# Kernel tuning notes

Hardware: AMD Instinct MI355X
Metric: run time of the kernel (lower is better)

The kernel has to match this reference:

```python
import jax, jax.numpy as jnp
import numpy as np

B, T, C = 8, 1024, 1024
H, HS = 16, 64            # n_head, head_size
K, STRIDE = 32, 16        # block_length, stride_length
WIN = 128                 # local_window_size
EPS = 1e-5


def _ln(z, w):
    m = jnp.mean(z, axis=-1, keepdims=True)
    v = jnp.var(z, axis=-1, keepdims=True)
    return (z - m) / jnp.sqrt(v + EPS) * w


def setup_inputs() -> dict:
    key = jax.random.key(0)
    ks = jax.random.split(key, 8)
    s = 0.02
    return {
        "x": jax.random.normal(ks[0], (B, T, C), jnp.float32),
        "c_attn_w": jax.random.normal(ks[1], (3 * C, C), jnp.float32) * s,
        "conv_w": jax.random.normal(ks[2], (HS, HS, K), jnp.float32) * s,
        "ln_comp_w": jnp.ones((HS,), jnp.float32),
        "ln_local_w": jnp.ones((C,), jnp.float32),
        "gate_w1": jax.random.normal(ks[3], (C, 2 * C), jnp.float32) * s,
        "gate_ln_w": jnp.ones((C,), jnp.float32),
        "gate_w2": jax.random.normal(ks[4], (2, C), jnp.float32) * s,
        "c_proj_w": jax.random.normal(ks[5], (C, C), jnp.float32) * s,
    }


def reference(x, c_attn_w, conv_w, ln_comp_w, ln_local_w, gate_w1, gate_ln_w, gate_w2, c_proj_w):
    qkv = jnp.einsum('btc,oc->bto', x, c_attn_w)          # [B,T,3C]
    q, k, v = jnp.split(qkv, 3, axis=-1)
    def heads(t):
        return t.reshape(B, T, H, HS).transpose(0, 2, 1, 3)  # [B,H,T,hs]
    q, k, v = heads(q), heads(k), heads(v)

    # CompressionMLP: Conv1d over time + LayerNorm(hs) + exact GELU
    def compress(t):
        xr = t.transpose(0, 1, 3, 2).reshape(B * H, HS, T)   # [B*H, hs, T]
        co = jax.lax.conv_general_dilated(
            xr, conv_w, window_strides=(STRIDE,), padding='VALID',
            dimension_numbers=('NCH', 'OIH', 'NCH'))          # [B*H, hs, NB]
        co = co.transpose(0, 2, 1)                            # [B*H, NB, hs]
        co = jax.nn.gelu(_ln(co, ln_comp_w), approximate=False)
        nb = co.shape[1]
        return co.reshape(B, H, nb, HS)

    kc = compress(k)
    vc = compress(v)
    NB = kc.shape[2]  # 63
    scale = 1.0 / np.sqrt(HS)

    ti = jnp.arange(T)
    band = (ti[None, :] <= ti[:, None]) & (ti[None, :] >= ti[:, None] - WIN)  # [T,T]
    s_loc = jnp.einsum('bhqd,bhkd->bhqk', q, k) * scale
    s_loc = jnp.where(band[None, None], s_loc, -jnp.inf)
    local_out = jnp.einsum('bhqk,bhkd->bhqd', jax.nn.softmax(s_loc, axis=-1), v)
    local_out = local_out.transpose(0, 2, 1, 3).reshape(B, T, C)
    local_norm = _ln(local_out, ln_local_w)

    # compressed-KV attention with block-causal mask: block j <= token i
    bj = jnp.arange(NB)
    cmask = bj[None, :] <= ti[:, None]                        # [T,NB]
    s_cmp = jnp.einsum('bhqd,bhkd->bhqk', q, kc) * scale
    s_cmp = jnp.where(cmask[None, None], s_cmp, -jnp.inf)
    comp_out = jnp.einsum('bhqk,bhkd->bhqd', jax.nn.softmax(s_cmp, axis=-1), vc)
    comp_out = comp_out.transpose(0, 2, 1, 3).reshape(B, T, C)

    # AttentionGating: last-token features -> Linear -> LN -> ReLU -> Linear -> softmax
    feats = jnp.concatenate([local_norm[:, -1, :], comp_out[:, -1, :]], axis=-1)  # [B,2C]
    h = jax.nn.relu(_ln(feats @ gate_w1.T, gate_ln_w))
    gates = jax.nn.softmax(h @ gate_w2.T, axis=-1)            # [B,2]

    combined = gates[:, None, 0:1] * local_norm + gates[:, None, 1:2] * comp_out
    y = jnp.einsum('btc,oc->bto', combined, c_proj_w)
    return y
```

## Files before the change

### kernel.cpp

```cpp
#include <hip/hip_runtime.h>
#include <cstdint>
#include <cmath>
#include <cstddef>

typedef unsigned int u32;
typedef unsigned short u16;
typedef __bf16 bf16x8 __attribute__((ext_vector_type(8)));
typedef float f32x4 __attribute__((ext_vector_type(4)));
typedef u32 u32x4 __attribute__((ext_vector_type(4)));
typedef u32 u32x2 __attribute__((ext_vector_type(2)));

#define DEV static __device__ __forceinline__

DEV u16 f2bf(float f) {
  u32 u = __float_as_uint(f);
  u += 0x7fffu + ((u >> 16) & 1u);
  return (u16)(u >> 16);
}
DEV float wredsum(float v) {
#pragma unroll
  for (int o = 32; o; o >>= 1) v += __shfl_xor(v, o, 64);
  return v;
}

DEV void gload_lds16(const u16* g, u16* lds_base) {
  __builtin_amdgcn_global_load_lds((const __attribute__((address_space(1))) void*)g,
                                   (__attribute__((address_space(3))) void*)lds_base,
                                   16, 0, 0);
}

__global__ __launch_bounds__(256) void cast_f32_bf16(const float* __restrict__ in,
                                                     u16* __restrict__ out) {
  const size_t idx = ((size_t)blockIdx.x * 256 + threadIdx.x) * 4;
  const f32x4 v = *(const f32x4*)&in[idx];
  u32x2 r;
  r[0] = (u32)f2bf(v[0]) | ((u32)f2bf(v[1]) << 16);
  r[1] = (u32)f2bf(v[2]) | ((u32)f2bf(v[3]) << 16);
  *(u32x2*)&out[idx] = r;
}

__global__ __launch_bounds__(256) void cast_convw(const float* __restrict__ cw,
                                                  u16* __restrict__ wc) {
  const int idx = blockIdx.x * 256 + threadIdx.x;
  const int o = idx >> 11;
  const int rest = idx & 2047;
  const int i = rest >> 5;
  const int kk = rest & 31;
  wc[(o << 11) + (kk << 6) + i] = f2bf(cw[idx]);
}

template <int OUT_BF16>
__global__ __launch_bounds__(256) void gemm_bt(const u16* __restrict__ A,
                                               const u16* __restrict__ Bm,
                                               void* __restrict__ out,
                                               int M, int N, int K) {
  __shared__ u16 As[128 * 32];
  __shared__ u16 Bs[128 * 32];
  const int tid = threadIdx.x;
  const int lane = tid & 63;
  const int w = tid >> 6;
  const int row0 = blockIdx.x * 128;
  const int col0 = blockIdx.y * 128;
  const int wm = (w >> 1) * 64, wn = (w & 1) * 64;
  const int lr = lane & 15, lq = lane >> 4;
  const int srow = lane >> 2;
  const int scol = (lane & 3) * 8;

  f32x4 acc[4][4] = {};

  for (int k0 = 0; k0 < K; k0 += 32) {
    __syncthreads();
#pragma unroll
    for (int p = 0; p < 2; ++p) {
      const int base_r = p * 64 + w * 16;
      gload_lds16(&A[(size_t)(row0 + base_r + srow) * K + k0 + scol], &As[base_r * 32]);
      gload_lds16(&Bm[(size_t)(col0 + base_r + srow) * K + k0 + scol], &Bs[base_r * 32]);
    }
    __syncthreads();
    bf16x8 af[4], bfr[4];
#pragma unroll
    for (int i = 0; i < 4; ++i) {
      af[i] = *(const bf16x8*)&As[(wm + i * 16 + lr) * 32 + lq * 8];
      bfr[i] = *(const bf16x8*)&Bs[(wn + i * 16 + lr) * 32 + lq * 8];
    }
#pragma unroll
    for (int i = 0; i < 4; ++i)
#pragma unroll
      for (int j = 0; j < 4; ++j)
        acc[i][j] = __builtin_amdgcn_mfma_f32_16x16x32_bf16(af[i], bfr[j], acc[i][j], 0, 0, 0);
  }
#pragma unroll
  for (int i = 0; i < 4; ++i)
#pragma unroll
    for (int j = 0; j < 4; ++j)
#pragma unroll
      for (int rr = 0; rr < 4; ++rr) {
        const int gr = row0 + wm + i * 16 + lq * 4 + rr;
        const int gc = col0 + wn + j * 16 + lr;
        const float v = acc[i][j][rr];
        if (OUT_BF16)
          ((u16*)out)[(size_t)gr * N + gc] = f2bf(v);
        else
          ((float*)out)[(size_t)gr * N + gc] = v;
      }
}

__global__ __launch_bounds__(256) void compress_kernel(const u16* __restrict__ qkv,
                                                       const u16* __restrict__ Wc,
                                                       const float* __restrict__ ln_w,
                                                       float* __restrict__ out_k,
                                                       float* __restrict__ out_v) {
  __shared__ u16 As[128 * 32];
  __shared__ u16 Bs[64 * 32];
  __shared__ float Cs[128][65];
  const int srcoff = 1024 + (int)blockIdx.y * 1024;
  float* outp = blockIdx.y ? out_v : out_k;
  const int tid = threadIdx.x;
  const int lane = tid & 63;
  const int w = tid >> 6;
  const int r0 = blockIdx.x * 128;
  const int lr = lane & 15, lq = lane >> 4;

  size_t rowbase[2];
#pragma unroll
  for (int p = 0; p < 2; ++p) {
    const int idx = p * 256 + tid;
    const int r = idx >> 2, c = (idx & 3) * 8;
    const int gr = r0 + r;
    const int bh = gr / 63;
    const int nb = gr - bh * 63;
    const int b = bh >> 4, h = bh & 15;
    rowbase[p] = (size_t)(b * 1024 + nb * 16) * 3072 + srcoff + h * 64 + c;
  }
  const int brow = tid >> 2, bcol = (tid & 3) * 8;

  f32x4 acc[2][4] = {};
  for (int k0 = 0; k0 < 2048; k0 += 32) {
    const int kk = k0 >> 6;
    const int i0 = k0 & 63;
    __syncthreads();
#pragma unroll
    for (int p = 0; p < 2; ++p) {
      const int idx = p * 256 + tid;
      const int r = idx >> 2, c = (idx & 3) * 8;
      *(u32x4*)&As[r * 32 + c] = *(const u32x4*)&qkv[rowbase[p] + (size_t)kk * 3072 + i0];
    }
    *(u32x4*)&Bs[brow * 32 + bcol] = *(const u32x4*)&Wc[(size_t)brow * 2048 + k0 + bcol];
    __syncthreads();
    bf16x8 af[2], bfr[4];
#pragma unroll
    for (int i = 0; i < 2; ++i) af[i] = *(const bf16x8*)&As[(w * 32 + i * 16 + lr) * 32 + lq * 8];
#pragma unroll
    for (int j = 0; j < 4; ++j) bfr[j] = *(const bf16x8*)&Bs[(j * 16 + lr) * 32 + lq * 8];
#pragma unroll
    for (int i = 0; i < 2; ++i)
#pragma unroll
      for (int j = 0; j < 4; ++j)
        acc[i][j] = __builtin_amdgcn_mfma_f32_16x16x32_bf16(af[i], bfr[j], acc[i][j], 0, 0, 0);
  }
  __syncthreads();
#pragma unroll
  for (int i = 0; i < 2; ++i)
#pragma unroll
    for (int j = 0; j < 4; ++j)
#pragma unroll
      for (int rr = 0; rr < 4; ++rr)
        Cs[w * 32 + i * 16 + lq * 4 + rr][j * 16 + lr] = acc[i][j][rr];
  __syncthreads();
  if (tid < 128) {
    const int r = tid;
    float s = 0.f, s2 = 0.f;
#pragma unroll 8
    for (int d = 0; d < 64; ++d) {
      const float x = Cs[r][d];
      s += x;
      s2 += x * x;
    }
    const float m = s * (1.f / 64.f);
    const float inv = rsqrtf(s2 * (1.f / 64.f) - m * m + 1e-5f);
    const size_t gr = (size_t)(r0 + r) * 64;
#pragma unroll 8
    for (int d = 0; d < 64; ++d) {
      const float z = (Cs[r][d] - m) * inv * ln_w[d];
      outp[gr + d] = 0.5f * z * (1.f + erff(z * 0.70710678118f));
    }
  }
}

__global__ __launch_bounds__(256) void local_attn(const u16* __restrict__ qkv,
                                                  float* __restrict__ loc) {
  __shared__ __align__(16) char smem[53248];
  u16* Ks = (u16*)smem;
  u16* Vt = (u16*)smem;
  u16* Ps = (u16*)(smem + 27648);
  const int bh = blockIdx.x;
  const int b = bh >> 4, h = bh & 15;
  const int i0 = blockIdx.y * 64;
  const int jbase = i0 - 128;
  const int tid = threadIdx.x;
  const int lane = tid & 63, w = tid >> 6;
  const int lr = lane & 15, lq = lane >> 4;

  u32x4 vreg[6];
#pragma unroll
  for (int c = 0; c < 6; ++c) {
    const int lin = c * 256 + tid;
    const int s = lin >> 3, d0 = (lin & 7) * 8;
    const int j = jbase + s;
    u32x4 kval = {0, 0, 0, 0}, vval = {0, 0, 0, 0};
    if (j >= 0) {
      const size_t ro = (size_t)(b * 1024 + j) * 3072 + h * 64 + d0;
      kval = *(const u32x4*)&qkv[ro + 1024];
      vval = *(const u32x4*)&qkv[ro + 2048];
    }
    vreg[c] = vval;
    *(u32x4*)&Ks[s * 72 + d0] = kval;
  }
  bf16x8 qf[2];
  {
    const size_t qrow = (size_t)(b * 1024 + i0 + w * 16 + lr) * 3072 + h * 64;
#pragma unroll
    for (int ks = 0; ks < 2; ++ks) qf[ks] = *(const bf16x8*)&qkv[qrow + ks * 32 + lq * 8];
  }
  __syncthreads();

  f32x4 sa[12];
#pragma unroll
  for (int j = 0; j < 12; ++j) sa[j] = (f32x4){0.f, 0.f, 0.f, 0.f};
#pragma unroll
  for (int ks = 0; ks < 2; ++ks)
#pragma unroll
    for (int j = 0; j < 12; ++j) {
      const bf16x8 kf = *(const bf16x8*)&Ks[(j * 16 + lr) * 72 + ks * 32 + lq * 8];
      sa[j] = __builtin_amdgcn_mfma_f32_16x16x32_bf16(qf[ks], kf, sa[j], 0, 0, 0);
    }

  const float NINF = -__builtin_inff();
  float mx[4] = {NINF, NINF, NINF, NINF};
#pragma unroll
  for (int j = 0; j < 12; ++j) {
    const int s = j * 16 + lr;
#pragma unroll
    for (int rr = 0; rr < 4; ++rr) {
      const int qi = w * 16 + lq * 4 + rr;
      const bool valid = (jbase + s >= 0) && (s >= qi) && (s <= qi + 128);
      const float v = valid ? sa[j][rr] * 0.125f : NINF;
      sa[j][rr] = v;
      mx[rr] = fmaxf(mx[rr], v);
    }
  }
#pragma unroll
  for (int rr = 0; rr < 4; ++rr)
#pragma unroll
    for (int o = 1; o < 16; o <<= 1) mx[rr] = fmaxf(mx[rr], __shfl_xor(mx[rr], o, 64));
  float sum[4] = {0.f, 0.f, 0.f, 0.f};
#pragma unroll
  for (int j = 0; j < 12; ++j)
#pragma unroll
    for (int rr = 0; rr < 4; ++rr) {
      const float p = __expf(sa[j][rr] - mx[rr]);
      sa[j][rr] = p;
      sum[rr] += p;
    }
#pragma unroll
  for (int rr = 0; rr < 4; ++rr) {
#pragma unroll
    for (int o = 1; o < 16; o <<= 1) sum[rr] += __shfl_xor(sum[rr], o, 64);
    sum[rr] = 1.0f / sum[rr];
  }
  __syncthreads();

#pragma unroll
  for (int j = 0; j < 12; ++j)
#pragma unroll
    for (int rr = 0; rr < 4; ++rr)
      Ps[(w * 16 + lq * 4 + rr) * 200 + j * 16 + lr] = f2bf(sa[j][rr] * sum[rr]);
#pragma unroll
  for (int c = 0; c < 6; ++c) {
    const int lin = c * 256 + tid;
    const int s = lin >> 3, d0 = (lin & 7) * 8;
    const u32x4 val = vreg[c];
#pragma unroll
    for (int q = 0; q < 4; ++q) {
      Vt[(d0 + 2 * q) * 200 + s] = (u16)(val[q] & 0xffffu);
      Vt[(d0 + 2 * q + 1) * 200 + s] = (u16)(val[q] >> 16);
    }
  }
  __syncthreads();

  f32x4 oa[4];
#pragma unroll
  for (int jt = 0; jt < 4; ++jt) oa[jt] = (f32x4){0.f, 0.f, 0.f, 0.f};
#pragma unroll
  for (int ks = 0; ks < 6; ++ks) {
    const bf16x8 pf = *(const bf16x8*)&Ps[(w * 16 + lr) * 200 + ks * 32 + lq * 8];
#pragma unroll
    for (int jt = 0; jt < 4; ++jt) {
      const bf16x8 vf = *(const bf16x8*)&Vt[(jt * 16 + lr) * 200 + ks * 32 + lq * 8];
      oa[jt] = __builtin_amdgcn_mfma_f32_16x16x32_bf16(pf, vf, oa[jt], 0, 0, 0);
    }
  }
#pragma unroll
  for (int jt = 0; jt < 4; ++jt)
#pragma unroll
    for (int rr = 0; rr < 4; ++rr)
      loc[(size_t)(b * 1024 + i0 + w * 16 + lq * 4 + rr) * 1024 + h * 64 + jt * 16 + lr] =
          oa[jt][rr];
}

__global__ __launch_bounds__(256) void comp_attn(const u16* __restrict__ qkv,
                                                 const float* __restrict__ kc,
                                                 const float* __restrict__ vc,
                                                 float* __restrict__ outc) {
  __shared__ u16 Kc[64 * 72];
  __shared__ u16 Vt[64 * 72];
  __shared__ u16 Ps[64 * 72];
  const int bh = blockIdx.x;
  const int b = bh >> 4, h = bh & 15;
  const int i0 = blockIdx.y * 64;
  const int tid = threadIdx.x;
  const int lane = tid & 63, w = tid >> 6;
  const int lr = lane & 15, lq = lane >> 4;
  const size_t kbase = (size_t)bh * 63 * 64;

  for (int idx = tid; idx < 63 * 64; idx += 256) {
    const int j = idx >> 6, d = idx & 63;
    Kc[j * 72 + d] = f2bf(kc[kbase + idx]);
    Vt[d * 72 + j] = f2bf(vc[kbase + idx]);
  }
  if (tid < 64) {
    Kc[63 * 72 + tid] = 0;
    Vt[tid * 72 + 63] = 0;
  }
  bf16x8 qf[2];
  {
    const size_t qrow = (size_t)(b * 1024 + i0 + w * 16 + lr) * 3072 + h * 64;
#pragma unroll
    for (int ks = 0; ks < 2; ++ks) qf[ks] = *(const bf16x8*)&qkv[qrow + ks * 32 + lq * 8];
  }
  __syncthreads();

  f32x4 sa[4];
#pragma unroll
  for (int j = 0; j < 4; ++j) sa[j] = (f32x4){0.f, 0.f, 0.f, 0.f};
#pragma unroll
  for (int ks = 0; ks < 2; ++ks)
#pragma unroll
    for (int j = 0; j < 4; ++j) {
      const bf16x8 kf = *(const bf16x8*)&Kc[(j * 16 + lr) * 72 + ks * 32 + lq * 8];
      sa[j] = __builtin_amdgcn_mfma_f32_16x16x32_bf16(qf[ks], kf, sa[j], 0, 0, 0);
    }

  const float NINF = -__builtin_inff();
  float mx[4] = {NINF, NINF, NINF, NINF};
#pragma unroll
  for (int j = 0; j < 4; ++j) {
    const int s = j * 16 + lr;
#pragma unroll
    for (int rr = 0; rr < 4; ++rr) {
      const int i = i0 + w * 16 + lq * 4 + rr;
      const bool valid = (s <= i) && (s < 63);
      const float v = valid ? sa[j][rr] * 0.125f : NINF;
      sa[j][rr] = v;
      mx[rr] = fmaxf(mx[rr], v);
    }
  }
#pragma unroll
  for (int rr = 0; rr < 4; ++rr)
#pragma unroll
    for (int o = 1; o < 16; o <<= 1) mx[rr] = fmaxf(mx[rr], __shfl_xor(mx[rr], o, 64));
  float sum[4] = {0.f, 0.f, 0.f, 0.f};
#pragma unroll
  for (int j = 0; j < 4; ++j)
#pragma unroll
    for (int rr = 0; rr < 4; ++rr) {
      const float p = __expf(sa[j][rr] - mx[rr]);
      sa[j][rr] = p;
      sum[rr] += p;
    }
#pragma unroll
  for (int rr = 0; rr < 4; ++rr) {
#pragma unroll
    for (int o = 1; o < 16; o <<= 1) sum[rr] += __shfl_xor(sum[rr], o, 64);
    sum[rr] = 1.0f / sum[rr];
  }
#pragma unroll
  for (int j = 0; j < 4; ++j)
#pragma unroll
    for (int rr = 0; rr < 4; ++rr)
      Ps[(w * 16 + lq * 4 + rr) * 72 + j * 16 + lr] = f2bf(sa[j][rr] * sum[rr]);
  __syncthreads();

  f32x4 oa[4];
#pragma unroll
  for (int jt = 0; jt < 4; ++jt) oa[jt] = (f32x4){0.f, 0.f, 0.f, 0.f};
#pragma unroll
  for (int ks = 0; ks < 2; ++ks) {
    const bf16x8 pf = *(const bf16x8*)&Ps[(w * 16 + lr) * 72 + ks * 32 + lq * 8];
#pragma unroll
    for (int jt = 0; jt < 4; ++jt) {
      const bf16x8 vf = *(const bf16x8*)&Vt[(jt * 16 + lr) * 72 + ks * 32 + lq * 8];
      oa[jt] = __builtin_amdgcn_mfma_f32_16x16x32_bf16(pf, vf, oa[jt], 0, 0, 0);
    }
  }
#pragma unroll
  for (int jt = 0; jt < 4; ++jt)
#pragma unroll
    for (int rr = 0; rr < 4; ++rr)
      outc[(size_t)(b * 1024 + i0 + w * 16 + lq * 4 + rr) * 1024 + h * 64 + jt * 16 + lr] =
          oa[jt][rr];
}

__global__ __launch_bounds__(256) void ln_feats(const float* __restrict__ locn,
                                                const float* __restrict__ comp,
                                                const float* __restrict__ lnw,
                                                float* __restrict__ feats) {
  const int b = blockIdx.x, tid = threadIdx.x;
  const size_t base = ((size_t)b * 1024 + 1023) * 1024 + tid * 4;
  const f32x4 v = *(const f32x4*)&locn[base];
  float s = v[0] + v[1] + v[2] + v[3];
  float s2 = v[0] * v[0] + v[1] * v[1] + v[2] * v[2] + v[3] * v[3];
  s = wredsum(s);
  s2 = wredsum(s2);
  __shared__ float rs[4], rs2[4];
  const int w = tid >> 6, lane = tid & 63;
  if (!lane) { rs[w] = s; rs2[w] = s2; }
  __syncthreads();
  s = rs[0] + rs[1] + rs[2] + rs[3];
  s2 = rs2[0] + rs2[1] + rs2[2] + rs2[3];
  const float m = s * (1.f / 1024.f);
  const float inv = rsqrtf(s2 * (1.f / 1024.f) - m * m + 1e-5f);
  const f32x4 wv = *(const f32x4*)&lnw[tid * 4];
  f32x4 o;
#pragma unroll
  for (int k = 0; k < 4; ++k) o[k] = (v[k] - m) * inv * wv[k];
  *(f32x4*)&feats[b * 2048 + tid * 4] = o;
  *(f32x4*)&feats[b * 2048 + 1024 + tid * 4] = *(const f32x4*)&comp[base];
}

__global__ __launch_bounds__(256) void gate_gemv(const float* __restrict__ feats,
                                                 const float* __restrict__ w1,
                                                 float* __restrict__ hraw) {
  const int o = blockIdx.x * 4 + (threadIdx.x >> 6);
  const int lane = threadIdx.x & 63;
  const float* wr = &w1[(size_t)o * 2048];
  float acc[8] = {};
#pragma unroll
  for (int it = 0; it < 8; ++it) {
    const int c = (it * 64 + lane) * 4;
    const f32x4 wv = *(const f32x4*)&wr[c];
#pragma unroll
    for (int b = 0; b < 8; ++b) {
      const f32x4 fv = *(const f32x4*)&feats[b * 2048 + c];
      acc[b] += fv[0] * wv[0] + fv[1] * wv[1] + fv[2] * wv[2] + fv[3] * wv[3];
    }
  }
#pragma unroll
  for (int b = 0; b < 8; ++b) acc[b] = wredsum(acc[b]);
  if (lane == 0) {
#pragma unroll
    for (int b = 0; b < 8; ++b) hraw[b * 1024 + o] = acc[b];
  }
}

__global__ __launch_bounds__(256) void gate_fin(const float* __restrict__ hraw,
                                                const float* __restrict__ lnw,
                                                const float* __restrict__ w2,
                                                float* __restrict__ gates) {
  const int b = blockIdx.x, tid = threadIdx.x;
  const f32x4 v = *(const f32x4*)&hraw[(size_t)b * 1024 + tid * 4];
  float s = v[0] + v[1] + v[2] + v[3];
  float s2 = v[0] * v[0] + v[1] * v[1] + v[2] * v[2] + v[3] * v[3];
  s = wredsum(s);
  s2 = wredsum(s2);
  __shared__ float rs[4], rs2[4];
  const int w = tid >> 6, lane = tid & 63;
  if (!lane) { rs[w] = s; rs2[w] = s2; }
  __syncthreads();
  s = rs[0] + rs[1] + rs[2] + rs[3];
  s2 = rs2[0] + rs2[1] + rs2[2] + rs2[3];
  const float m = s * (1.f / 1024.f);
  const float inv = rsqrtf(s2 * (1.f / 1024.f) - m * m + 1e-5f);
  float p0 = 0.f, p1 = 0.f;
#pragma unroll
  for (int k = 0; k < 4; ++k) {
    float hh = (v[k] - m) * inv * lnw[tid * 4 + k];
    hh = fmaxf(hh, 0.f);
    p0 += hh * w2[tid * 4 + k];
    p1 += hh * w2[1024 + tid * 4 + k];
  }
  p0 = wredsum(p0);
  p1 = wredsum(p1);
  __syncthreads();
  if (!lane) { rs[w] = p0; rs2[w] = p1; }
  __syncthreads();
  if (tid == 0) {
    const float l0 = rs[0] + rs[1] + rs[2] + rs[3];
    const float l1 = rs2[0] + rs2[1] + rs2[2] + rs2[3];
    const float mm = fmaxf(l0, l1);
    const float e0 = __expf(l0 - mm), e1 = __expf(l1 - mm);
    const float iv = 1.f / (e0 + e1);
    gates[b * 2] = e0 * iv;
    gates[b * 2 + 1] = e1 * iv;
  }
}

__global__ __launch_bounds__(256) void combine_ln_cast(const float* __restrict__ locn,
                                                       const float* __restrict__ comp,
                                                       const float* __restrict__ lnw,
                                                       const float* __restrict__ gates,
                                                       u16* __restrict__ outb) {
  const int row = blockIdx.x, tid = threadIdx.x;
  const size_t base = (size_t)row * 1024 + tid * 4;
  const f32x4 v = *(const f32x4*)&locn[base];
  float s = v[0] + v[1] + v[2] + v[3];
  float s2 = v[0] * v[0] + v[1] * v[1] + v[2] * v[2] + v[3] * v[3];
  s = wredsum(s);
  s2 = wredsum(s2);
  __shared__ float rs[4], rs2[4];
  const int w = tid >> 6, lane = tid & 63;
  if (!lane) { rs[w] = s; rs2[w] = s2; }
  __syncthreads();
  s = rs[0] + rs[1] + rs[2] + rs[3];
  s2 = rs2[0] + rs2[1] + rs2[2] + rs2[3];
  const float m = s * (1.f / 1024.f);
  const float inv = rsqrtf(s2 * (1.f / 1024.f) - m * m + 1e-5f);
  const int b = row >> 10;
  const float g0 = gates[2 * b], g1 = gates[2 * b + 1];
  const f32x4 wv = *(const f32x4*)&lnw[tid * 4];
  const f32x4 c = *(const f32x4*)&comp[base];
  float ov[4];
#pragma unroll
  for (int k = 0; k < 4; ++k) ov[k] = g0 * ((v[k] - m) * inv * wv[k]) + g1 * c[k];
  u32x2 r;
  r[0] = (u32)f2bf(ov[0]) | ((u32)f2bf(ov[1]) << 16);
  r[1] = (u32)f2bf(ov[2]) | ((u32)f2bf(ov[3]) << 16);
  *(u32x2*)&outb[base] = r;
}

extern "C" void kernel_launch(void* const* d_in, const int* in_sizes, int n_in,
                              void* d_out, int out_size, void* d_ws, size_t ws_size,
                              hipStream_t stream) {
  const float* x = (const float*)d_in[0];
  const float* c_attn_w = (const float*)d_in[1];
  const float* conv_w = (const float*)d_in[2];
  const float* ln_comp_w = (const float*)d_in[3];
  const float* ln_local_w = (const float*)d_in[4];
  const float* gate_w1 = (const float*)d_in[5];
  const float* gate_ln_w = (const float*)d_in[6];
  const float* gate_w2 = (const float*)d_in[7];
  const float* c_proj_w = (const float*)d_in[8];
  float* y = (float*)d_out;

  char* ws = (char*)d_ws;
  size_t off = 0;
  auto alloc = [&](size_t bytes) -> void* {
    void* p = ws + off;
    off += (bytes + 255) & ~(size_t)255;
    return p;
  };
  u16* qkvb = (u16*)alloc((size_t)8192 * 3072 * 2);
  u16* xb = (u16*)alloc((size_t)8192 * 1024 * 2);
  u16* wab = (u16*)alloc((size_t)3072 * 1024 * 2);
  u16* wpb = (u16*)alloc((size_t)1024 * 1024 * 2);
  u16* wcb = (u16*)alloc((size_t)64 * 2048 * 2);
  float* kc = (float*)alloc((size_t)8064 * 64 * 4);
  float* vc = (float*)alloc((size_t)8064 * 64 * 4);
  float* locn = (float*)alloc((size_t)8192 * 1024 * 4);
  float* comp = (float*)alloc((size_t)8192 * 1024 * 4);
  float* feats = (float*)alloc((size_t)8 * 2048 * 4);
  float* hraw = (float*)alloc((size_t)8192 * 4);
  float* gates = (float*)alloc(64);
  u16* combb = (u16*)alloc((size_t)8192 * 1024 * 2);

  cast_f32_bf16<<<8192, 256, 0, stream>>>(x, xb);
  cast_f32_bf16<<<3072, 256, 0, stream>>>(c_attn_w, wab);
  cast_f32_bf16<<<1024, 256, 0, stream>>>(c_proj_w, wpb);
  cast_convw<<<512, 256, 0, stream>>>(conv_w, wcb);

  gemm_bt<1><<<dim3(64, 24), 256, 0, stream>>>(xb, wab, qkvb, 8192, 3072, 1024);

  compress_kernel<<<dim3(63, 2), 256, 0, stream>>>(qkvb, wcb, ln_comp_w, kc, vc);

  local_attn<<<dim3(128, 16), 256, 0, stream>>>(qkvb, locn);
  comp_attn<<<dim3(128, 16), 256, 0, stream>>>(qkvb, kc, vc, comp);

  ln_feats<<<8, 256, 0, stream>>>(locn, comp, ln_local_w, feats);
  gate_gemv<<<256, 256, 0, stream>>>(feats, gate_w1, hraw);
  gate_fin<<<8, 256, 0, stream>>>(hraw, gate_ln_w, gate_w2, gates);

  combine_ln_cast<<<8192, 256, 0, stream>>>(locn, comp, ln_local_w, gates, combb);

  gemm_bt<0><<<dim3(64, 8), 256, 0, stream>>>(combb, wpb, y, 8192, 1024, 1024);
}
```

Before: 333.0 us.

## Fuse local and compressed attention, store intermediates in bf16, skip masked tiles

Merges the four cast kernels into one launch, which also zero-pads the compressed K/V buffers. The compress kernel now writes bf16 compressed K and transposed V directly. The local and compressed attention kernels are fused so each block reuses its Q fragments. The local score loop computes only the 9 key tiles inside each wave's band instead of 12, and the PV loop does 5 k-steps instead of 6. Local and compressed attention outputs are stored as bf16 instead of fp32, which halves traffic into the gating and combine kernels at some cost in precision.

```diff
diff --git a/kernel.cpp b/kernel.cpp
--- a/kernel.cpp
+++ b/kernel.cpp
@@ -12,11 +12,16 @@
 
 #define DEV static __device__ __forceinline__
 
+DEV float bflo(u32 u) { return __uint_as_float(u << 16); }
+DEV float bfhi(u32 u) { return __uint_as_float(u & 0xffff0000u); }
 DEV u16 f2bf(float f) {
   u32 u = __float_as_uint(f);
   u += 0x7fffu + ((u >> 16) & 1u);
   return (u16)(u >> 16);
 }
+DEV f32x4 unpack_bf4(u32x2 r) {
+  return (f32x4){bflo(r[0]), bfhi(r[0]), bflo(r[1]), bfhi(r[1])};
+}
 DEV float wredsum(float v) {
 #pragma unroll
   for (int o = 32; o; o >>= 1) v += __shfl_xor(v, o, 64);
@@ -29,24 +34,44 @@
                                    16, 0, 0);
 }
 
-__global__ __launch_bounds__(256) void cast_f32_bf16(const float* __restrict__ in,
-                                                     u16* __restrict__ out) {
-  const size_t idx = ((size_t)blockIdx.x * 256 + threadIdx.x) * 4;
-  const f32x4 v = *(const f32x4*)&in[idx];
-  u32x2 r;
-  r[0] = (u32)f2bf(v[0]) | ((u32)f2bf(v[1]) << 16);
-  r[1] = (u32)f2bf(v[2]) | ((u32)f2bf(v[3]) << 16);
-  *(u32x2*)&out[idx] = r;
-}
-
-__global__ __launch_bounds__(256) void cast_convw(const float* __restrict__ cw,
-                                                  u16* __restrict__ wc) {
-  const int idx = blockIdx.x * 256 + threadIdx.x;
-  const int o = idx >> 11;
-  const int rest = idx & 2047;
-  const int i = rest >> 5;
-  const int kk = rest & 31;
-  wc[(o << 11) + (kk << 6) + i] = f2bf(cw[idx]);
+__global__ __launch_bounds__(256) void fused_cast(const float* __restrict__ x,
+                                                  const float* __restrict__ aw,
+                                                  const float* __restrict__ pw,
+                                                  const float* __restrict__ cw,
+                                                  u16* __restrict__ xb,
+                                                  u16* __restrict__ wab,
+                                                  u16* __restrict__ wpb,
+                                                  u16* __restrict__ wcb,
+                                                  u16* __restrict__ kcb,
+                                                  u16* __restrict__ vcb) {
+  const int blk = blockIdx.x;
+  if (blk < 12288) {
+    const float* src;
+    u16* dst;
+    int base;
+    if (blk < 8192) { src = x; dst = xb; base = blk; }
+    else if (blk < 11264) { src = aw; dst = wab; base = blk - 8192; }
+    else { src = pw; dst = wpb; base = blk - 11264; }
+    const size_t idx = ((size_t)base * 256 + threadIdx.x) * 4;
+    const f32x4 v = *(const f32x4*)&src[idx];
+    u32x2 r;
+    r[0] = (u32)f2bf(v[0]) | ((u32)f2bf(v[1]) << 16);
+    r[1] = (u32)f2bf(v[2]) | ((u32)f2bf(v[3]) << 16);
+    *(u32x2*)&dst[idx] = r;
+  } else if (blk < 12800) {
+    const int idx = (blk - 12288) * 256 + threadIdx.x;
+    const int o = idx >> 11;
+    const int rest = idx & 2047;
+    const int i = rest >> 5;
+    const int kk = rest & 31;
+    wcb[(o << 11) + (kk << 6) + i] = f2bf(cw[idx]);
+  } else {
+    for (int i = threadIdx.x; i < 8192; i += 256) {
+      const int bh = i >> 6, d = i & 63;
+      kcb[bh * 4096 + 63 * 64 + d] = 0;
+      vcb[bh * 4096 + d * 64 + 63] = 0;
+    }
+  }
 }
 
 template <int OUT_BF16>
@@ -108,13 +133,12 @@
 __global__ __launch_bounds__(256) void compress_kernel(const u16* __restrict__ qkv,
                                                        const u16* __restrict__ Wc,
                                                        const float* __restrict__ ln_w,
-                                                       float* __restrict__ out_k,
-                                                       float* __restrict__ out_v) {
+                                                       u16* __restrict__ kcb,
+                                                       u16* __restrict__ vcb) {
   __shared__ u16 As[128 * 32];
   __shared__ u16 Bs[64 * 32];
   __shared__ float Cs[128][65];
   const int srcoff = 1024 + (int)blockIdx.y * 1024;
-  float* outp = blockIdx.y ? out_v : out_k;
   const int tid = threadIdx.x;
   const int lane = tid & 63;
   const int w = tid >> 6;
@@ -169,26 +193,41 @@
   __syncthreads();
   if (tid < 128) {
     const int r = tid;
+    const int gr = r0 + r;
+    const int bh2 = gr / 63;
+    const int nb2 = gr - bh2 * 63;
     float s = 0.f, s2 = 0.f;
 #pragma unroll 8
     for (int d = 0; d < 64; ++d) {
-      const float x = Cs[r][d];
-      s += x;
-      s2 += x * x;
+      const float xv = Cs[r][d];
+      s += xv;
+      s2 += xv * xv;
     }
     const float m = s * (1.f / 64.f);
     const float inv = rsqrtf(s2 * (1.f / 64.f) - m * m + 1e-5f);
-    const size_t gr = (size_t)(r0 + r) * 64;
+    if (blockIdx.y == 0) {
+      const size_t gb = (size_t)bh2 * 4096 + nb2 * 64;
 #pragma unroll 8
-    for (int d = 0; d < 64; ++d) {
-      const float z = (Cs[r][d] - m) * inv * ln_w[d];
-      outp[gr + d] = 0.5f * z * (1.f + erff(z * 0.70710678118f));
-    }
-  }
-}
-
-__global__ __launch_bounds__(256) void local_attn(const u16* __restrict__ qkv,
-                                                  float* __restrict__ loc) {
+      for (int d = 0; d < 64; ++d) {
+        const float z = (Cs[r][d] - m) * inv * ln_w[d];
+        kcb[gb + d] = f2bf(0.5f * z * (1.f + erff(z * 0.70710678118f)));
+      }
+    } else {
+      const size_t gb = (size_t)bh2 * 4096 + nb2;
+#pragma unroll 8
+      for (int d = 0; d < 64; ++d) {
+        const float z = (Cs[r][d] - m) * inv * ln_w[d];
+        vcb[gb + d * 64] = f2bf(0.5f * z * (1.f + erff(z * 0.70710678118f)));
+      }
+    }
+  }
+}
+
+__global__ __launch_bounds__(256) void attn_fused(const u16* __restrict__ qkv,
+                                                  const u16* __restrict__ kcb,
+                                                  const u16* __restrict__ vcb,
+                                                  u16* __restrict__ loc,
+                                                  u16* __restrict__ outc) {
   __shared__ __align__(16) char smem[53248];
   u16* Ks = (u16*)smem;
   u16* Vt = (u16*)smem;
@@ -224,28 +263,29 @@
   }
   __syncthreads();
 
-  f32x4 sa[12];
-#pragma unroll
-  for (int j = 0; j < 12; ++j) sa[j] = (f32x4){0.f, 0.f, 0.f, 0.f};
+  f32x4 sa[9];
+#pragma unroll
+  for (int j9 = 0; j9 < 9; ++j9) sa[j9] = (f32x4){0.f, 0.f, 0.f, 0.f};
 #pragma unroll
   for (int ks = 0; ks < 2; ++ks)
 #pragma unroll
-    for (int j = 0; j < 12; ++j) {
-      const bf16x8 kf = *(const bf16x8*)&Ks[(j * 16 + lr) * 72 + ks * 32 + lq * 8];
-      sa[j] = __builtin_amdgcn_mfma_f32_16x16x32_bf16(qf[ks], kf, sa[j], 0, 0, 0);
+    for (int j9 = 0; j9 < 9; ++j9) {
+      const int jt = w + j9;
+      const bf16x8 kf = *(const bf16x8*)&Ks[(jt * 16 + lr) * 72 + ks * 32 + lq * 8];
+      sa[j9] = __builtin_amdgcn_mfma_f32_16x16x32_bf16(qf[ks], kf, sa[j9], 0, 0, 0);
     }
 
   const float NINF = -__builtin_inff();
   float mx[4] = {NINF, NINF, NINF, NINF};
 #pragma unroll
-  for (int j = 0; j < 12; ++j) {
-    const int s = j * 16 + lr;
+  for (int j9 = 0; j9 < 9; ++j9) {
+    const int s = (w + j9) * 16 + lr;
 #pragma unroll
     for (int rr = 0; rr < 4; ++rr) {
       const int qi = w * 16 + lq * 4 + rr;
       const bool valid = (jbase + s >= 0) && (s >= qi) && (s <= qi + 128);
-      const float v = valid ? sa[j][rr] * 0.125f : NINF;
-      sa[j][rr] = v;
+      const float v = valid ? sa[j9][rr] * 0.125f : NINF;
+      sa[j9][rr] = v;
       mx[rr] = fmaxf(mx[rr], v);
     }
   }
@@ -255,11 +295,11 @@
     for (int o = 1; o < 16; o <<= 1) mx[rr] = fmaxf(mx[rr], __shfl_xor(mx[rr], o, 64));
   float sum[4] = {0.f, 0.f, 0.f, 0.f};
 #pragma unroll
-  for (int j = 0; j < 12; ++j)
+  for (int j9 = 0; j9 < 9; ++j9)
 #pragma unroll
     for (int rr = 0; rr < 4; ++rr) {
-      const float p = __expf(sa[j][rr] - mx[rr]);
-      sa[j][rr] = p;
+      const float p = __expf(sa[j9][rr] - mx[rr]);
+      sa[j9][rr] = p;
       sum[rr] += p;
     }
 #pragma unroll
@@ -271,10 +311,17 @@
   __syncthreads();
 
 #pragma unroll
-  for (int j = 0; j < 12; ++j)
+  for (int j9 = 0; j9 < 9; ++j9) {
+    const int jt = w + j9;
 #pragma unroll
     for (int rr = 0; rr < 4; ++rr)
-      Ps[(w * 16 + lq * 4 + rr) * 200 + j * 16 + lr] = f2bf(sa[j][rr] * sum[rr]);
+      Ps[(w * 16 + lq * 4 + rr) * 200 + jt * 16 + lr] = f2bf(sa[j9][rr] * sum[rr]);
+  }
+  {
+    const int jz = (w == 0) ? 9 : (w == 1) ? 0 : (w == 2) ? 11 : 2;
+#pragma unroll
+    for (int rr = 0; rr < 4; ++rr) Ps[(w * 16 + lq * 4 + rr) * 200 + jz * 16 + lr] = 0;
+  }
 #pragma unroll
   for (int c = 0; c < 6; ++c) {
     const int lin = c * 256 + tid;
@@ -288,15 +335,16 @@
   }
   __syncthreads();
 
+  const int W = (w >> 1) * 32;
   f32x4 oa[4];
 #pragma unroll
   for (int jt = 0; jt < 4; ++jt) oa[jt] = (f32x4){0.f, 0.f, 0.f, 0.f};
 #pragma unroll
-  for (int ks = 0; ks < 6; ++ks) {
-    const bf16x8 pf = *(const bf16x8*)&Ps[(w * 16 + lr) * 200 + ks * 32 + lq * 8];
+  for (int ks = 0; ks < 5; ++ks) {
+    const bf16x8 pf = *(const bf16x8*)&Ps[(w * 16 + lr) * 200 + W + ks * 32 + lq * 8];
 #pragma unroll
     for (int jt = 0; jt < 4; ++jt) {
-      const bf16x8 vf = *(const bf16x8*)&Vt[(jt * 16 + lr) * 200 + ks * 32 + lq * 8];
+      const bf16x8 vf = *(const bf16x8*)&Vt[(jt * 16 + lr) * 200 + W + ks * 32 + lq * 8];
       oa[jt] = __builtin_amdgcn_mfma_f32_16x16x32_bf16(pf, vf, oa[jt], 0, 0, 0);
     }
   }
@@ -305,54 +353,34 @@
 #pragma unroll
     for (int rr = 0; rr < 4; ++rr)
       loc[(size_t)(b * 1024 + i0 + w * 16 + lq * 4 + rr) * 1024 + h * 64 + jt * 16 + lr] =
-          oa[jt][rr];
-}
-
-__global__ __launch_bounds__(256) void comp_attn(const u16* __restrict__ qkv,
-                                                 const float* __restrict__ kc,
-                                                 const float* __restrict__ vc,
-                                                 float* __restrict__ outc) {
-  __shared__ u16 Kc[64 * 72];
-  __shared__ u16 Vt[64 * 72];
-  __shared__ u16 Ps[64 * 72];
-  const int bh = blockIdx.x;
-  const int b = bh >> 4, h = bh & 15;
-  const int i0 = blockIdx.y * 64;
-  const int tid = threadIdx.x;
-  const int lane = tid & 63, w = tid >> 6;
-  const int lr = lane & 15, lq = lane >> 4;
-  const size_t kbase = (size_t)bh * 63 * 64;
-
-  for (int idx = tid; idx < 63 * 64; idx += 256) {
-    const int j = idx >> 6, d = idx & 63;
-    Kc[j * 72 + d] = f2bf(kc[kbase + idx]);
-    Vt[d * 72 + j] = f2bf(vc[kbase + idx]);
-  }
-  if (tid < 64) {
-    Kc[63 * 72 + tid] = 0;
-    Vt[tid * 72 + 63] = 0;
-  }
-  bf16x8 qf[2];
-  {
-    const size_t qrow = (size_t)(b * 1024 + i0 + w * 16 + lr) * 3072 + h * 64;
-#pragma unroll
-    for (int ks = 0; ks < 2; ++ks) qf[ks] = *(const bf16x8*)&qkv[qrow + ks * 32 + lq * 8];
-  }
-  __syncthreads();
-
-  f32x4 sa[4];
-#pragma unroll
-  for (int j = 0; j < 4; ++j) sa[j] = (f32x4){0.f, 0.f, 0.f, 0.f};
+          f2bf(oa[jt][rr]);
+
+  __syncthreads();
+  u16* Kc = (u16*)smem;
+  u16* Vc = (u16*)(smem + 9216);
+  u16* Pc = (u16*)(smem + 18432);
+  const size_t cb = (size_t)bh * 4096;
+  for (int c2 = tid; c2 < 512; c2 += 256) {
+    const int nb = c2 >> 3, d0 = (c2 & 7) * 8;
+    *(u32x4*)&Kc[nb * 72 + d0] = *(const u32x4*)&kcb[cb + nb * 64 + d0];
+  }
+  for (int c2 = tid; c2 < 512; c2 += 256) {
+    const int d = c2 >> 3, n0 = (c2 & 7) * 8;
+    *(u32x4*)&Vc[d * 72 + n0] = *(const u32x4*)&vcb[cb + d * 64 + n0];
+  }
+  __syncthreads();
+
+  f32x4 ca[4];
+#pragma unroll
+  for (int j = 0; j < 4; ++j) ca[j] = (f32x4){0.f, 0.f, 0.f, 0.f};
 #pragma unroll
   for (int ks = 0; ks < 2; ++ks)
 #pragma unroll
     for (int j = 0; j < 4; ++j) {
       const bf16x8 kf = *(const bf16x8*)&Kc[(j * 16 + lr) * 72 + ks * 32 + lq * 8];
-      sa[j] = __builtin_amdgcn_mfma_f32_16x16x32_bf16(qf[ks], kf, sa[j], 0, 0, 0);
-    }
-
-  const float NINF = -__builtin_inff();
-  float mx[4] = {NINF, NINF, NINF, NINF};
+      ca[j] = __builtin_amdgcn_mfma_f32_16x16x32_bf16(qf[ks], kf, ca[j], 0, 0, 0);
+    }
+  float mc[4] = {NINF, NINF, NINF, NINF};
 #pragma unroll
   for (int j = 0; j < 4; ++j) {
     const int s = j * 16 + lr;
@@ -360,47 +388,47 @@
     for (int rr = 0; rr < 4; ++rr) {
       const int i = i0 + w * 16 + lq * 4 + rr;
       const bool valid = (s <= i) && (s < 63);
-      const float v = valid ? sa[j][rr] * 0.125f : NINF;
-      sa[j][rr] = v;
-      mx[rr] = fmaxf(mx[rr], v);
+      const float v = valid ? ca[j][rr] * 0.125f : NINF;
+      ca[j][rr] = v;
+      mc[rr] = fmaxf(mc[rr], v);
     }
   }
 #pragma unroll
   for (int rr = 0; rr < 4; ++rr)
 #pragma unroll
-    for (int o = 1; o < 16; o <<= 1) mx[rr] = fmaxf(mx[rr], __shfl_xor(mx[rr], o, 64));
-  float sum[4] = {0.f, 0.f, 0.f, 0.f};
+    for (int o = 1; o < 16; o <<= 1) mc[rr] = fmaxf(mc[rr], __shfl_xor(mc[rr], o, 64));
+  float sc[4] = {0.f, 0.f, 0.f, 0.f};
 #pragma unroll
   for (int j = 0; j < 4; ++j)
 #pragma unroll
     for (int rr = 0; rr < 4; ++rr) {
-      const float p = __expf(sa[j][rr] - mx[rr]);
-      sa[j][rr] = p;
-      sum[rr] += p;
+      const float p = __expf(ca[j][rr] - mc[rr]);
+      ca[j][rr] = p;
+      sc[rr] += p;
     }
 #pragma unroll
   for (int rr = 0; rr < 4; ++rr) {
 #pragma unroll
-    for (int o = 1; o < 16; o <<= 1) sum[rr] += __shfl_xor(sum[rr], o, 64);
-    sum[rr] = 1.0f / sum[rr];
+    for (int o = 1; o < 16; o <<= 1) sc[rr] += __shfl_xor(sc[rr], o, 64);
+    sc[rr] = 1.0f / sc[rr];
   }
 #pragma unroll
   for (int j = 0; j < 4; ++j)
 #pragma unroll
     for (int rr = 0; rr < 4; ++rr)
-      Ps[(w * 16 + lq * 4 + rr) * 72 + j * 16 + lr] = f2bf(sa[j][rr] * sum[rr]);
-  __syncthreads();
-
-  f32x4 oa[4];
-#pragma unroll
-  for (int jt = 0; jt < 4; ++jt) oa[jt] = (f32x4){0.f, 0.f, 0.f, 0.f};
+      Pc[(w * 16 + lq * 4 + rr) * 72 + j * 16 + lr] = f2bf(ca[j][rr] * sc[rr]);
+  __syncthreads();
+
+  f32x4 co[4];
+#pragma unroll
+  for (int jt = 0; jt < 4; ++jt) co[jt] = (f32x4){0.f, 0.f, 0.f, 0.f};
 #pragma unroll
   for (int ks = 0; ks < 2; ++ks) {
-    const bf16x8 pf = *(const bf16x8*)&Ps[(w * 16 + lr) * 72 + ks * 32 + lq * 8];
+    const bf16x8 pf = *(const bf16x8*)&Pc[(w * 16 + lr) * 72 + ks * 32 + lq * 8];
 #pragma unroll
     for (int jt = 0; jt < 4; ++jt) {
-      const bf16x8 vf = *(const bf16x8*)&Vt[(jt * 16 + lr) * 72 + ks * 32 + lq * 8];
-      oa[jt] = __builtin_amdgcn_mfma_f32_16x16x32_bf16(pf, vf, oa[jt], 0, 0, 0);
+      const bf16x8 vf = *(const bf16x8*)&Vc[(jt * 16 + lr) * 72 + ks * 32 + lq * 8];
+      co[jt] = __builtin_amdgcn_mfma_f32_16x16x32_bf16(pf, vf, co[jt], 0, 0, 0);
     }
   }
 #pragma unroll
@@ -408,16 +436,16 @@
 #pragma unroll
     for (int rr = 0; rr < 4; ++rr)
       outc[(size_t)(b * 1024 + i0 + w * 16 + lq * 4 + rr) * 1024 + h * 64 + jt * 16 + lr] =
-          oa[jt][rr];
-}
-
-__global__ __launch_bounds__(256) void ln_feats(const float* __restrict__ locn,
-                                                const float* __restrict__ comp,
+          f2bf(co[jt][rr]);
+}
+
+__global__ __launch_bounds__(256) void ln_feats(const u16* __restrict__ locb,
+                                                const u16* __restrict__ compb,
                                                 const float* __restrict__ lnw,
                                                 float* __restrict__ feats) {
   const int b = blockIdx.x, tid = threadIdx.x;
   const size_t base = ((size_t)b * 1024 + 1023) * 1024 + tid * 4;
-  const f32x4 v = *(const f32x4*)&locn[base];
+  const f32x4 v = unpack_bf4(*(const u32x2*)&locb[base]);
   float s = v[0] + v[1] + v[2] + v[3];
   float s2 = v[0] * v[0] + v[1] * v[1] + v[2] * v[2] + v[3] * v[3];
   s = wredsum(s);
@@ -435,7 +463,7 @@
 #pragma unroll
   for (int k = 0; k < 4; ++k) o[k] = (v[k] - m) * inv * wv[k];
   *(f32x4*)&feats[b * 2048 + tid * 4] = o;
-  *(f32x4*)&feats[b * 2048 + 1024 + tid * 4] = *(const f32x4*)&comp[base];
+  *(f32x4*)&feats[b * 2048 + 1024 + tid * 4] = unpack_bf4(*(const u32x2*)&compb[base]);
 }
 
 __global__ __launch_bounds__(256) void gate_gemv(const float* __restrict__ feats,
@@ -505,14 +533,14 @@
   }
 }
 
-__global__ __launch_bounds__(256) void combine_ln_cast(const float* __restrict__ locn,
-                                                       const float* __restrict__ comp,
+__global__ __launch_bounds__(256) void combine_ln_cast(const u16* __restrict__ locb,
+                                                       const u16* __restrict__ compb,
                                                        const float* __restrict__ lnw,
                                                        const float* __restrict__ gates,
                                                        u16* __restrict__ outb) {
   const int row = blockIdx.x, tid = threadIdx.x;
   const size_t base = (size_t)row * 1024 + tid * 4;
-  const f32x4 v = *(const f32x4*)&locn[base];
+  const f32x4 v = unpack_bf4(*(const u32x2*)&locb[base]);
   float s = v[0] + v[1] + v[2] + v[3];
   float s2 = v[0] * v[0] + v[1] * v[1] + v[2] * v[2] + v[3] * v[3];
   s = wredsum(s);
@@ -528,7 +556,7 @@
   const int b = row >> 10;
   const float g0 = gates[2 * b], g1 = gates[2 * b + 1];
   const f32x4 wv = *(const f32x4*)&lnw[tid * 4];
-  const f32x4 c = *(const f32x4*)&comp[base];
+  const f32x4 c = unpack_bf4(*(const u32x2*)&compb[base]);
   float ov[4];
 #pragma unroll
   for (int k = 0; k < 4; ++k) ov[k] = g0 * ((v[k] - m) * inv * wv[k]) + g1 * c[k];
@@ -564,32 +592,29 @@
   u16* wab = (u16*)alloc((size_t)3072 * 1024 * 2);
   u16* wpb = (u16*)alloc((size_t)1024 * 1024 * 2);
   u16* wcb = (u16*)alloc((size_t)64 * 2048 * 2);
-  float* kc = (float*)alloc((size_t)8064 * 64 * 4);
-  float* vc = (float*)alloc((size_t)8064 * 64 * 4);
-  float* locn = (float*)alloc((size_t)8192 * 1024 * 4);
-  float* comp = (float*)alloc((size_t)8192 * 1024 * 4);
+  u16* kcb = (u16*)alloc((size_t)128 * 4096 * 2);
+  u16* vcb = (u16*)alloc((size_t)128 * 4096 * 2);
+  u16* locb = (u16*)alloc((size_t)8192 * 1024 * 2);
+  u16* compb = (u16*)alloc((size_t)8192 * 1024 * 2);
   float* feats = (float*)alloc((size_t)8 * 2048 * 4);
   float* hraw = (float*)alloc((size_t)8192 * 4);
   float* gates = (float*)alloc(64);
   u16* combb = (u16*)alloc((size_t)8192 * 1024 * 2);
 
-  cast_f32_bf16<<<8192, 256, 0, stream>>>(x, xb);
-  cast_f32_bf16<<<3072, 256, 0, stream>>>(c_attn_w, wab);
-  cast_f32_bf16<<<1024, 256, 0, stream>>>(c_proj_w, wpb);
-  cast_convw<<<512, 256, 0, stream>>>(conv_w, wcb);
+  fused_cast<<<12801, 256, 0, stream>>>(x, c_attn_w, c_proj_w, conv_w, xb, wab, wpb, wcb, kcb,
+                                        vcb);
 
   gemm_bt<1><<<dim3(64, 24), 256, 0, stream>>>(xb, wab, qkvb, 8192, 3072, 1024);
 
-  compress_kernel<<<dim3(63, 2), 256, 0, stream>>>(qkvb, wcb, ln_comp_w, kc, vc);
-
-  local_attn<<<dim3(128, 16), 256, 0, stream>>>(qkvb, locn);
-  comp_attn<<<dim3(128, 16), 256, 0, stream>>>(qkvb, kc, vc, comp);
-
-  ln_feats<<<8, 256, 0, stream>>>(locn, comp, ln_local_w, feats);
+  compress_kernel<<<dim3(63, 2), 256, 0, stream>>>(qkvb, wcb, ln_comp_w, kcb, vcb);
+
+  attn_fused<<<dim3(128, 16), 256, 0, stream>>>(qkvb, kcb, vcb, locb, compb);
+
+  ln_feats<<<8, 256, 0, stream>>>(locb, compb, ln_local_w, feats);
   gate_gemv<<<256, 256, 0, stream>>>(feats, gate_w1, hraw);
   gate_fin<<<8, 256, 0, stream>>>(hraw, gate_ln_w, gate_w2, gates);
 
-  combine_ln_cast<<<8192, 256, 0, stream>>>(locn, comp, ln_local_w, gates, combb);
+  combine_ln_cast<<<8192, 256, 0, stream>>>(locb, compb, ln_local_w, gates, combb);
 
   gemm_bt<0><<<dim3(64, 8), 256, 0, stream>>>(combb, wpb, y, 8192, 1024, 1024);
 }
```

After: 314.0 us. -5.7%, faster.
